# Kernel optimization log

Hardware: AMD Instinct MI355X
Metric: run time of the kernel (lower is better)

The kernel has to match this reference:

```python
import jax, jax.numpy as jnp
import numpy as np

HIDDEN = 2048
N_HEADS = 16
N_KV_HEADS = 8
HEAD_DIM = 128
MROPE_SECTION = [8, 8, 24, 24]          # sums to HEAD_DIM // 2
ROPE_THETA = 10000.0
B, S, CTX = 4, 1024, 2048
# per-frequency section index (which of the 4 position streams drives each freq)
_SEC_IDX = np.repeat(np.arange(len(MROPE_SECTION)), MROPE_SECTION)  # (HEAD_DIM//2,)


def setup_inputs() -> dict:
    key = jax.random.key(0)
    ks = jax.random.split(key, 6)
    return {
        "hidden_states": jax.random.normal(ks[0], (B, S, HIDDEN), jnp.float32),
        "Wqkv": jax.random.normal(ks[1], (HIDDEN, (N_HEADS + 2 * N_KV_HEADS) * HEAD_DIM), jnp.float32) * 0.02,
        "Wo": jax.random.normal(ks[2], (N_HEADS * HEAD_DIM, HIDDEN), jnp.float32) * 0.02,
        "ctx_k": jax.random.normal(ks[3], (B, CTX, N_KV_HEADS, HEAD_DIM), jnp.float32),
        "ctx_v": jax.random.normal(ks[4], (B, CTX, N_KV_HEADS, HEAD_DIM), jnp.float32),
        "position_ids": jax.random.randint(ks[5], (len(MROPE_SECTION), S), 0, CTX + S, jnp.int32),
    }


def _mrope_cos_sin(position_ids):
    # position_ids: (n_sections, S) int -> cos/sin of shape (S, HEAD_DIM)
    half = HEAD_DIM // 2
    inv_freq = 1.0 / (ROPE_THETA ** (jnp.arange(0, half, dtype=jnp.float32) * 2.0 / HEAD_DIM))
    freqs = position_ids.astype(jnp.float32)[:, :, None] * inv_freq[None, None, :]  # (4, S, half)
    sec = jnp.asarray(_SEC_IDX)[None, None, :]                                       # (1, 1, half)
    f = jnp.take_along_axis(freqs, jnp.broadcast_to(sec, (1,) + freqs.shape[1:]), axis=0)[0]  # (S, half)
    emb = jnp.concatenate([f, f], axis=-1)  # (S, HEAD_DIM)
    return jnp.cos(emb), jnp.sin(emb)


def _rotate_half(x):
    h = x.shape[-1] // 2
    return jnp.concatenate([-x[..., h:], x[..., :h]], axis=-1)


def reference(hidden_states, Wqkv, Wo, ctx_k, ctx_v, position_ids):
    b, s, _ = hidden_states.shape
    q_size = N_HEADS * HEAD_DIM
    kv_size = N_KV_HEADS * HEAD_DIM
    qkv = hidden_states @ Wqkv  # (B, S, q+2kv)
    q = qkv[..., :q_size].reshape(b, s, N_HEADS, HEAD_DIM)
    k = qkv[..., q_size:q_size + kv_size].reshape(b, s, N_KV_HEADS, HEAD_DIM)
    v = qkv[..., q_size + kv_size:].reshape(b, s, N_KV_HEADS, HEAD_DIM)

    cos, sin = _mrope_cos_sin(position_ids)        # (S, D) each
    cos = cos[None, :, None, :]
    sin = sin[None, :, None, :]
    q = q * cos + _rotate_half(q) * sin
    k = k * cos + _rotate_half(k) * sin

    # KV-cache concat along sequence dim
    k = jnp.concatenate([ctx_k, k], axis=1)        # (B, CTX+S, KV, D)
    v = jnp.concatenate([ctx_v, v], axis=1)

    # GQA: expand kv heads to query heads
    rep = N_HEADS // N_KV_HEADS
    k = jnp.repeat(k, rep, axis=2)                 # (B, T, H, D)
    v = jnp.repeat(v, rep, axis=2)

    scale = HEAD_DIM ** -0.5
    scores = jnp.einsum("bqhd,bkhd->bhqk", q, k) * scale  # non-causal
    probs = jax.nn.softmax(scores, axis=-1)
    out = jnp.einsum("bhqk,bkhd->bqhd", probs, v)  # (B, S, H, D)
    out = out.reshape(b, s, N_HEADS * HEAD_DIM)
    return out @ Wo
```

## Files before the change

### kernel.cpp

```cpp
#include <hip/hip_runtime.h>
#include <hip/hip_bf16.h>
#include <stdint.h>

#define NH 16
#define NKV 8
#define HD 128
#define BB 4
#define SS 1024
#define CTXL 2048
#define LT 3072
#define HID 2048
#define QKVN 4096
#define MROWS 4096

typedef __hip_bfloat16 bf16;
using f32x4 = __attribute__((ext_vector_type(4))) float;
using s16x8 = __attribute__((ext_vector_type(8))) short;

#define MFMA(a, b, c) __builtin_amdgcn_mfma_f32_16x16x32_bf16((a), (b), (c), 0, 0, 0)

__device__ __forceinline__ void gload_lds16(const void* g, void* l) {
  __builtin_amdgcn_global_load_lds((const __attribute__((address_space(1))) void*)g,
                                   (__attribute__((address_space(3))) void*)l, 16, 0, 0);
}

__device__ __forceinline__ void store_bf8(bf16* dst, const float* f) {
  bf16 tmp[8];
#pragma unroll
  for (int j = 0; j < 8; ++j) tmp[j] = __float2bfloat16(f[j]);
  __builtin_memcpy((void*)dst, (const void*)tmp, 16);
}

__device__ __forceinline__ float bf2f(short x) {
  unsigned int u = ((unsigned int)(unsigned short)x) << 16;
  float f;
  __builtin_memcpy(&f, &u, 4);
  return f;
}

#define P1_CVT 4096
#define P1_WQ (P1_CVT + 8192)
#define P1_WO (P1_WQ + 4096)
#define P1_RT (P1_WO + 256)
#define P1_CK (P1_RT + 4096)
#define P1_CV (P1_CK + 8192)

__global__ void prep1(const float* __restrict__ hs, const float* __restrict__ Wqkv,
                      const float* __restrict__ Wo, const float* __restrict__ ck,
                      const float* __restrict__ cv, const int* __restrict__ pid,
                      bf16* __restrict__ Hb, bf16* __restrict__ WqT,
                      bf16* __restrict__ WoT, bf16* __restrict__ Kf,
                      bf16* __restrict__ Vt, float* __restrict__ cosT,
                      float* __restrict__ sinT) {
  __shared__ float tile[32][33];
  const int blk = blockIdx.x, thr = threadIdx.x;
  if (blk < P1_CVT) {
    size_t tid = (size_t)blk * 256 + thr;
    const float4* p = (const float4*)(hs + tid * 8);
    float4 a = p[0], b = p[1];
    float f[8] = {a.x, a.y, a.z, a.w, b.x, b.y, b.z, b.w};
    store_bf8(Hb + tid * 8, f);
  } else if (blk < P1_WQ) {
    int j = blk - P1_CVT;
    int c0 = (j & 127) * 32, r0 = (j >> 7) * 32;
    int tx = thr & 31, ty = thr >> 5;
#pragma unroll
    for (int i = 0; i < 32; i += 8)
      tile[ty + i][tx] = Wqkv[(size_t)(r0 + ty + i) * QKVN + c0 + tx];
    __syncthreads();
#pragma unroll
    for (int i = 0; i < 32; i += 8)
      WqT[(size_t)(c0 + ty + i) * HID + r0 + tx] = __float2bfloat16(tile[tx][ty + i]);
  } else if (blk < P1_WO) {
    int j = blk - P1_WQ;
    int c0 = (j & 63) * 32, r0 = (j >> 6) * 32;
    int tx = thr & 31, ty = thr >> 5;
#pragma unroll
    for (int i = 0; i < 32; i += 8)
      tile[ty + i][tx] = Wo[(size_t)(r0 + ty + i) * 2048 + c0 + tx];
    __syncthreads();
#pragma unroll
    for (int i = 0; i < 32; i += 8)
      WoT[(size_t)(c0 + ty + i) * 2048 + r0 + tx] = __float2bfloat16(tile[tx][ty + i]);
  } else if (blk < P1_RT) {
    int tid = (blk - P1_WO) * 256 + thr;
    int j = tid & 63, s = tid >> 6;
    int sec = (j < 8) ? 0 : (j < 16) ? 1 : (j < 40) ? 2 : 3;
    float pos = (float)pid[sec * SS + s];
    float inv = __expf(-(float)j * 0.14391156831212787f);
    float a = pos * inv;
    cosT[tid] = cosf(a);
    sinT[tid] = sinf(a);
  } else if (blk < P1_CK) {
    int tid = (blk - P1_RT) * 256 + thr;
    int d8 = tid & 15, l = (tid >> 4) & 2047, h = (tid >> 15) & 7, b = tid >> 18;
    const float* s = ck + (((size_t)b * CTXL + l) * NKV + h) * HD + d8 * 8;
    const float4* p = (const float4*)s;
    float4 a = p[0], bb = p[1];
    float f[8] = {a.x, a.y, a.z, a.w, bb.x, bb.y, bb.z, bb.w};
    store_bf8(Kf + (((size_t)(b * NKV + h)) * LT + l) * HD + d8 * 8, f);
  } else {
    int j = blk - P1_CK;
    int l0 = (j & 63) * 32, d0 = ((j >> 6) & 3) * 32;
    int bz = j >> 8, b = bz >> 3, h = bz & 7;
    int tx = thr & 31, ty = thr >> 5;
#pragma unroll
    for (int i = 0; i < 32; i += 8)
      tile[ty + i][tx] =
          cv[(((size_t)b * CTXL + l0 + ty + i) * NKV + h) * HD + d0 + tx];
    __syncthreads();
#pragma unroll
    for (int i = 0; i < 32; i += 8)
      Vt[(((size_t)(b * NKV + h)) * HD + d0 + ty + i) * LT + l0 + tx] =
          __float2bfloat16(tile[tx][ty + i]);
  }
}

__global__ void prep2(const bf16* __restrict__ qkv, const float* __restrict__ cosT,
                      const float* __restrict__ sinT, bf16* __restrict__ Kf,
                      bf16* __restrict__ Vt) {
  __shared__ float tile[32][33];
  const int blk = blockIdx.x, thr = threadIdx.x;
  if (blk < 8192) {
    int tid = blk * 256 + thr;
    int j = tid & 63, h = (tid >> 6) & 7, s = (tid >> 9) & 1023, b = tid >> 19;
    const bf16* src = qkv + ((size_t)b * SS + s) * QKVN + 2048 + h * HD;
    float x1 = __bfloat162float(src[j]), x2 = __bfloat162float(src[j + 64]);
    float c = cosT[s * 64 + j], sn = sinT[s * 64 + j];
    bf16* dst = Kf + (((size_t)(b * NKV + h)) * LT + CTXL + s) * HD;
    dst[j] = __float2bfloat16(x1 * c - x2 * sn);
    dst[j + 64] = __float2bfloat16(x2 * c + x1 * sn);
  } else {
    int j = blk - 8192;
    int s0 = (j & 31) * 32, d0 = ((j >> 5) & 3) * 32;
    int bz = j >> 7, b = bz >> 3, h = bz & 7;
    int tx = thr & 31, ty = thr >> 5;
#pragma unroll
    for (int i = 0; i < 32; i += 8)
      tile[ty + i][tx] = __bfloat162float(
          qkv[((size_t)b * SS + s0 + ty + i) * QKVN + 3072 + h * HD + d0 + tx]);
    __syncthreads();
#pragma unroll
    for (int i = 0; i < 32; i += 8)
      Vt[(((size_t)(b * NKV + h)) * HD + d0 + ty + i) * LT + CTXL + s0 + tx] =
          __float2bfloat16(tile[tx][ty + i]);
  }
}

template <typename OT>
__global__ __launch_bounds__(512, 1) void gemm_bt(const bf16* __restrict__ A,
                                                  const bf16* __restrict__ BT,
                                                  OT* __restrict__ C, int M, int N,
                                                  int K) {
  __shared__ __attribute__((aligned(16))) bf16 lA[3][256][64];
  __shared__ __attribute__((aligned(16))) bf16 lB[3][128][64];
  const int t = threadIdx.x;
  const int lane = t & 63, w = t >> 6;
  const int wr = w >> 1, wc = w & 1;
  const int lrow = lane & 15, kgrp = lane >> 4;
  const int rchk = lrow & 7;
  const int lin = blockIdx.y * gridDim.x + blockIdx.x;
  const int qq = (gridDim.x * gridDim.y) >> 3;
  const int swz = (lin & 7) * qq + (lin >> 3);
  const int bx = swz % gridDim.x, by = swz / gridDim.x;
  const int m0 = by * 256, n0 = bx * 128;
  const int srow = lane >> 3;
  const int schk = (lane & 7) ^ srow;
  const f32x4 fz = {0.f, 0.f, 0.f, 0.f};
  f32x4 acc[4][4];
#pragma unroll
  for (int i = 0; i < 4; ++i)
#pragma unroll
    for (int j = 0; j < 4; ++j) acc[i][j] = fz;
  const int NTK = K >> 6;

#define GSTAGE(ib, kt)                                                      \
  do {                                                                      \
    _Pragma("unroll") for (int c = 0; c < 4; ++c) {                         \
      int ra = c * 64 + w * 8 + srow;                                       \
      gload_lds16(A + (size_t)(m0 + ra) * K + (kt)*64 + schk * 8,           \
                  &lA[ib][c * 64 + w * 8][0]);                              \
    }                                                                       \
    _Pragma("unroll") for (int c = 0; c < 2; ++c) {                         \
      int rb = c * 64 + w * 8 + srow;                                       \
      gload_lds16(BT + (size_t)(n0 + rb) * K + (kt)*64 + schk * 8,          \
                  &lB[ib][c * 64 + w * 8][0]);                              \
    }                                                                       \
  } while (0)

  GSTAGE(0, 0);
  GSTAGE(1, 1);
  int ib = 0;
  for (int kt = 0; kt < NTK; ++kt) {
    if (kt + 1 < NTK)
      asm volatile("s_waitcnt vmcnt(6) lgkmcnt(0)" ::: "memory");
    else
      asm volatile("s_waitcnt vmcnt(0) lgkmcnt(0)" ::: "memory");
    __builtin_amdgcn_s_barrier();
    __builtin_amdgcn_sched_barrier(0);
    if (kt + 2 < NTK) {
      int ib2 = ib + 2;
      if (ib2 >= 3) ib2 -= 3;
      GSTAGE(ib2, kt + 2);
    }
#pragma unroll
    for (int kk = 0; kk < 2; ++kk) {
      s16x8 af[4], bf[4];
#pragma unroll
      for (int i = 0; i < 4; ++i)
        af[i] = *(const s16x8*)&lA[ib][wr * 64 + i * 16 + lrow]
                                     [(((kk << 2) + kgrp) ^ rchk) * 8];
#pragma unroll
      for (int j = 0; j < 4; ++j)
        bf[j] = *(const s16x8*)&lB[ib][wc * 64 + j * 16 + lrow]
                                     [(((kk << 2) + kgrp) ^ rchk) * 8];
      __builtin_amdgcn_s_setprio(1);
#pragma unroll
      for (int i = 0; i < 4; ++i)
#pragma unroll
        for (int j = 0; j < 4; ++j) acc[i][j] = MFMA(af[i], bf[j], acc[i][j]);
      __builtin_amdgcn_s_setprio(0);
    }
    ++ib;
    if (ib >= 3) ib = 0;
  }
#undef GSTAGE

#pragma unroll
  for (int i = 0; i < 4; ++i)
#pragma unroll
    for (int j = 0; j < 4; ++j)
#pragma unroll
      for (int r = 0; r < 4; ++r) {
        int row = m0 + wr * 64 + i * 16 + kgrp * 4 + r;
        int col = n0 + wc * 64 + j * 16 + lrow;
        float v = acc[i][j][r];
        if constexpr (sizeof(OT) == 2)
          C[(size_t)row * N + col] = __float2bfloat16(v);
        else
          C[(size_t)row * N + col] = v;
      }
}


#define PSTR 72
#define KVB 128
#define NTT 24
#define SCALE2 0.1275174335919605f

__global__ __launch_bounds__(512, 2) void flash_attn(
    const bf16* __restrict__ qkv, const float* __restrict__ cosT,
    const float* __restrict__ sinT, const bf16* __restrict__ Kf,
    const bf16* __restrict__ Vt, bf16* __restrict__ O) {
  __shared__ __attribute__((aligned(16))) bf16 Kl[2][128][128];
  __shared__ __attribute__((aligned(16))) bf16 Vl[128][128];
  __shared__ __attribute__((aligned(16))) bf16 P_lds[8][32][PSTR];
  const int t = threadIdx.x, lane = t & 63, w = t >> 6;
  const int id = blockIdx.x;
  const int b = id >> 6, hk = id & 7;
  const int h = (hk << 1) | ((id >> 5) & 1);
  const int qb = (id >> 3) & 3;
  const int lrow = lane & 15, kgrp = lane >> 4;
  const bf16* Kp = Kf + (size_t)(b * NKV + hk) * LT * HD;
  const bf16* Vp = Vt + (size_t)(b * NKV + hk) * HD * LT;

  s16x8 qf[2][4];
#pragma unroll
  for (int f = 0; f < 2; ++f) {
    int srw_i = qb * 256 + w * 32 + f * 16 + lrow;
    const bf16* qrow = qkv + ((size_t)b * SS + srw_i) * QKVN + h * HD;
    s16x8 qr[4];
#pragma unroll
    for (int kd = 0; kd < 4; ++kd)
      qr[kd] = *(const s16x8*)&qrow[kd * 32 + kgrp * 8];
    const float* crow = cosT + srw_i * 64 + kgrp * 8;
    const float* srow = sinT + srw_i * 64 + kgrp * 8;
    float qv[4][8], cc[2][8], ssv[2][8];
#pragma unroll
    for (int kd = 0; kd < 4; ++kd)
#pragma unroll
      for (int j = 0; j < 8; ++j) qv[kd][j] = bf2f(qr[kd][j]);
#pragma unroll
    for (int g = 0; g < 2; ++g)
#pragma unroll
      for (int j = 0; j < 8; ++j) {
        cc[g][j] = crow[g * 32 + j];
        ssv[g][j] = srow[g * 32 + j];
      }
    bf16 o[4][8];
#pragma unroll
    for (int j = 0; j < 8; ++j) {
      o[0][j] = __float2bfloat16(qv[0][j] * cc[0][j] - qv[2][j] * ssv[0][j]);
      o[1][j] = __float2bfloat16(qv[1][j] * cc[1][j] - qv[3][j] * ssv[1][j]);
      o[2][j] = __float2bfloat16(qv[2][j] * cc[0][j] + qv[0][j] * ssv[0][j]);
      o[3][j] = __float2bfloat16(qv[3][j] * cc[1][j] + qv[1][j] * ssv[1][j]);
    }
#pragma unroll
    for (int kd = 0; kd < 4; ++kd) __builtin_memcpy(&qf[f][kd], o[kd], 16);
  }

  const f32x4 fz = {0.f, 0.f, 0.f, 0.f};
  f32x4 acc[2][8];
#pragma unroll
  for (int f = 0; f < 2; ++f)
#pragma unroll
    for (int i = 0; i < 8; ++i) acc[f][i] = fz;
  float m_[2] = {-1e30f, -1e30f}, l_[2] = {0.f, 0.f};

#define STAGE_K(buf, l0)                                                        \
  do {                                                                          \
    _Pragma("unroll") for (int c = 0; c < 4; ++c) {                             \
      int row = w * 16 + c * 4 + (lane >> 4);                                   \
      gload_lds16(Kp + (size_t)((l0) + row) * HD + ((lane & 15) ^ (row & 15)) * 8, \
                  &Kl[buf][w * 16 + c * 4][0]);                                 \
    }                                                                           \
  } while (0)
#define STAGE_V(l0)                                                             \
  do {                                                                          \
    _Pragma("unroll") for (int c = 0; c < 4; ++c) {                             \
      int d = w * 16 + c * 4 + (lane >> 4);                                     \
      gload_lds16(Vp + (size_t)d * LT + (l0) + ((lane & 15) ^ (d & 15)) * 8,    \
                  &Vl[w * 16 + c * 4][0]);                                      \
    }                                                                           \
  } while (0)

  STAGE_K(0, 0);
  __syncthreads();

  for (int tt = 0; tt < NTT; ++tt) {
    const int cur = tt & 1;
    STAGE_V(tt * KVB);
    if (tt + 1 < NTT) STAGE_K(cur ^ 1, (tt + 1) * KVB);

    f32x4 sc[2][8];
#pragma unroll
    for (int f = 0; f < 2; ++f)
#pragma unroll
      for (int cf = 0; cf < 8; ++cf) sc[f][cf] = fz;
#pragma unroll
    for (int cf = 0; cf < 8; ++cf)
#pragma unroll
      for (int kd = 0; kd < 4; ++kd) {
        s16x8 kb =
            *(const s16x8*)&Kl[cur][cf * 16 + lrow][((kd * 4 + kgrp) ^ lrow) * 8];
#pragma unroll
        for (int f = 0; f < 2; ++f) sc[f][cf] = MFMA(kb, qf[f][kd], sc[f][cf]);
      }

    float mxv[2];
#pragma unroll
    for (int f = 0; f < 2; ++f) {
      float mx = sc[f][0][0];
#pragma unroll
      for (int cf = 0; cf < 8; ++cf)
#pragma unroll
        for (int r = 0; r < 4; ++r) mx = fmaxf(mx, sc[f][cf][r]);
      mx *= SCALE2;
      mx = fmaxf(mx, __shfl_xor(mx, 16, 64));
      mx = fmaxf(mx, __shfl_xor(mx, 32, 64));
      mxv[f] = mx;
    }
    bool nb = (mxv[0] > m_[0] + 8.f) || (mxv[1] > m_[1] + 8.f);
    if (__any(nb)) {
#pragma unroll
      for (int f = 0; f < 2; ++f) {
        float mn = fmaxf(m_[f], mxv[f]);
        float so = exp2f(m_[f] - mn);
        m_[f] = mn;
        l_[f] *= so;
        float sob[4];
#pragma unroll
        for (int r = 0; r < 4; ++r) sob[r] = __shfl(so, kgrp * 4 + r, 16);
#pragma unroll
        for (int nd = 0; nd < 8; ++nd)
#pragma unroll
          for (int r = 0; r < 4; ++r) acc[f][nd][r] *= sob[r];
      }
    }

    float lp[2] = {0.f, 0.f};
#pragma unroll
    for (int f = 0; f < 2; ++f)
#pragma unroll
      for (int cf = 0; cf < 4; ++cf) {
        bf16 pk[4];
#pragma unroll
        for (int r = 0; r < 4; ++r) {
          float p = exp2f(sc[f][cf][r] * SCALE2 - m_[f]);
          lp[f] += p;
          pk[r] = __float2bfloat16(p);
        }
        __builtin_memcpy((void*)&P_lds[w][f * 16 + lrow][cf * 16 + kgrp * 4], pk, 8);
      }
    s16x8 pa[2][2];
#pragma unroll
    for (int f = 0; f < 2; ++f)
#pragma unroll
      for (int kc = 0; kc < 2; ++kc)
        pa[f][kc] = *(const s16x8*)&P_lds[w][f * 16 + lrow][kc * 32 + kgrp * 8];

    __syncthreads();

#pragma unroll
    for (int nd = 0; nd < 8; ++nd)
#pragma unroll
      for (int kc = 0; kc < 2; ++kc) {
        s16x8 vb = *(const s16x8*)&Vl[nd * 16 + lrow]
                                     [((kc * 4 + kgrp) ^ lrow) * 8];
#pragma unroll
        for (int f = 0; f < 2; ++f) acc[f][nd] = MFMA(pa[f][kc], vb, acc[f][nd]);
      }

#pragma unroll
    for (int f = 0; f < 2; ++f)
#pragma unroll
      for (int cf = 4; cf < 8; ++cf) {
        bf16 pk[4];
#pragma unroll
        for (int r = 0; r < 4; ++r) {
          float p = exp2f(sc[f][cf][r] * SCALE2 - m_[f]);
          lp[f] += p;
          pk[r] = __float2bfloat16(p);
        }
        __builtin_memcpy(
            (void*)&P_lds[w][f * 16 + lrow][(cf - 4) * 16 + kgrp * 4], pk, 8);
      }
#pragma unroll
    for (int f = 0; f < 2; ++f) {
      l_[f] += lp[f];
#pragma unroll
      for (int kc = 0; kc < 2; ++kc)
        pa[f][kc] = *(const s16x8*)&P_lds[w][f * 16 + lrow][kc * 32 + kgrp * 8];
    }
#pragma unroll
    for (int nd = 0; nd < 8; ++nd)
#pragma unroll
      for (int kc = 0; kc < 2; ++kc) {
        s16x8 vb = *(const s16x8*)&Vl[nd * 16 + lrow]
                                     [((8 + kc * 4 + kgrp) ^ lrow) * 8];
#pragma unroll
        for (int f = 0; f < 2; ++f) acc[f][nd] = MFMA(pa[f][kc], vb, acc[f][nd]);
      }
    __syncthreads();
  }
#undef STAGE_K
#undef STAGE_V

  float li[2][4];
#pragma unroll
  for (int f = 0; f < 2; ++f) {
    float lv = l_[f];
    lv += __shfl_xor(lv, 16, 64);
    lv += __shfl_xor(lv, 32, 64);
#pragma unroll
    for (int r = 0; r < 4; ++r) li[f][r] = 1.f / __shfl(lv, kgrp * 4 + r, 16);
  }
#pragma unroll
  for (int f = 0; f < 2; ++f)
#pragma unroll
    for (int nd = 0; nd < 8; ++nd)
#pragma unroll
      for (int r = 0; r < 4; ++r) {
        int row = qb * 256 + w * 32 + f * 16 + kgrp * 4 + r;
        O[((size_t)b * SS + row) * 2048 + h * HD + nd * 16 + lrow] =
            __float2bfloat16(acc[f][nd][r] * li[f][r]);
      }
}


extern "C" void kernel_launch(void* const* d_in, const int* in_sizes, int n_in,
                              void* d_out, int out_size, void* d_ws, size_t ws_size,
                              hipStream_t stream) {
  const float* hs = (const float*)d_in[0];
  const float* Wqkv = (const float*)d_in[1];
  const float* Wo = (const float*)d_in[2];
  const float* ctx_k = (const float*)d_in[3];
  const float* ctx_v = (const float*)d_in[4];
  const int* pid = (const int*)d_in[5];
  float* out = (float*)d_out;
  char* ws = (char*)d_ws;

  bf16* Hb = (bf16*)(ws);
  bf16* WqT = (bf16*)(ws + 16777216);
  bf16* WoT = (bf16*)(ws + 33554432);
  bf16* qkv = (bf16*)(ws + 41943040);
  bf16* Kfull = (bf16*)(ws + 92274688);
  bf16* Vt = (bf16*)(ws + 117440512);
  float* cosT = (float*)(ws + 142606336);
  float* sinT = (float*)(ws + 142606336 + 262144);
  bf16* attn = Hb;

  prep1<<<P1_CV, 256, 0, stream>>>(hs, Wqkv, Wo, ctx_k, ctx_v, pid, Hb, WqT, WoT,
                                   Kfull, Vt, cosT, sinT);
  gemm_bt<bf16><<<dim3(QKVN / 128, MROWS / 256), 512, 0, stream>>>(
      Hb, WqT, qkv, MROWS, QKVN, HID);
  prep2<<<12288, 256, 0, stream>>>(qkv, cosT, sinT, Kfull, Vt);
  flash_attn<<<256, 512, 0, stream>>>(qkv, cosT, sinT, Kfull, Vt, attn);
  gemm_bt<float><<<dim3(2048 / 128, MROWS / 256), 512, 0, stream>>>(
      attn, WoT, out, MROWS, 2048, HID);
}
```

Before: 325.8 us.

## Double-buffer V tiles and drop mid-iteration barrier in flash attention

V tiles now get their own double buffer in LDS and are prefetched one iteration ahead together with K, instead of being loaded at the start of the iteration that uses them. Because the current V tile is already resident, the `__syncthreads` between the two P·V halves is removed, and the two halves are folded into one loop. P staging is shrunk to one 16-row slab per wave, reused for both query fragments. This aims to hide V load latency and cut a block-wide barrier per tile, at the cost of a larger LDS footprint (about 146KB) that leaves little headroom.

```diff
diff --git a/kernel.cpp b/kernel.cpp
--- a/kernel.cpp
+++ b/kernel.cpp
@@ -253,8 +253,8 @@
     const float* __restrict__ sinT, const bf16* __restrict__ Kf,
     const bf16* __restrict__ Vt, bf16* __restrict__ O) {
   __shared__ __attribute__((aligned(16))) bf16 Kl[2][128][128];
-  __shared__ __attribute__((aligned(16))) bf16 Vl[128][128];
-  __shared__ __attribute__((aligned(16))) bf16 P_lds[8][32][PSTR];
+  __shared__ __attribute__((aligned(16))) bf16 Vl[2][128][128];
+  __shared__ __attribute__((aligned(16))) bf16 P_lds[8][16][PSTR];
   const int t = threadIdx.x, lane = t & 63, w = t >> 6;
   const int id = blockIdx.x;
   const int b = id >> 6, hk = id & 7;
@@ -315,22 +315,25 @@
                   &Kl[buf][w * 16 + c * 4][0]);                                 \
     }                                                                           \
   } while (0)
-#define STAGE_V(l0)                                                             \
+#define STAGE_V(buf, l0)                                                        \
   do {                                                                          \
     _Pragma("unroll") for (int c = 0; c < 4; ++c) {                             \
       int d = w * 16 + c * 4 + (lane >> 4);                                     \
       gload_lds16(Vp + (size_t)d * LT + (l0) + ((lane & 15) ^ (d & 15)) * 8,    \
-                  &Vl[w * 16 + c * 4][0]);                                      \
+                  &Vl[buf][w * 16 + c * 4][0]);                                 \
     }                                                                           \
   } while (0)
 
   STAGE_K(0, 0);
+  STAGE_V(0, 0);
   __syncthreads();
 
   for (int tt = 0; tt < NTT; ++tt) {
     const int cur = tt & 1;
-    STAGE_V(tt * KVB);
-    if (tt + 1 < NTT) STAGE_K(cur ^ 1, (tt + 1) * KVB);
+    if (tt + 1 < NTT) {
+      STAGE_K(cur ^ 1, (tt + 1) * KVB);
+      STAGE_V(cur ^ 1, (tt + 1) * KVB);
+    }
 
     f32x4 sc[2][8];
 #pragma unroll
@@ -380,67 +383,39 @@
 
     float lp[2] = {0.f, 0.f};
 #pragma unroll
-    for (int f = 0; f < 2; ++f)
-#pragma unroll
-      for (int cf = 0; cf < 4; ++cf) {
-        bf16 pk[4];
-#pragma unroll
-        for (int r = 0; r < 4; ++r) {
-          float p = exp2f(sc[f][cf][r] * SCALE2 - m_[f]);
-          lp[f] += p;
-          pk[r] = __float2bfloat16(p);
+    for (int half = 0; half < 2; ++half) {
+      s16x8 pa[2][2];
+#pragma unroll
+      for (int f = 0; f < 2; ++f) {
+#pragma unroll
+        for (int cf = 0; cf < 4; ++cf) {
+          int cfs = half * 4 + cf;
+          bf16 pk[4];
+#pragma unroll
+          for (int r = 0; r < 4; ++r) {
+            float p = exp2f(sc[f][cfs][r] * SCALE2 - m_[f]);
+            lp[f] += p;
+            pk[r] = __float2bfloat16(p);
+          }
+          __builtin_memcpy((void*)&P_lds[w][lrow][cf * 16 + kgrp * 4], pk, 8);
         }
-        __builtin_memcpy((void*)&P_lds[w][f * 16 + lrow][cf * 16 + kgrp * 4], pk, 8);
-      }
-    s16x8 pa[2][2];
-#pragma unroll
-    for (int f = 0; f < 2; ++f)
-#pragma unroll
-      for (int kc = 0; kc < 2; ++kc)
-        pa[f][kc] = *(const s16x8*)&P_lds[w][f * 16 + lrow][kc * 32 + kgrp * 8];
-
-    __syncthreads();
-
-#pragma unroll
-    for (int nd = 0; nd < 8; ++nd)
-#pragma unroll
-      for (int kc = 0; kc < 2; ++kc) {
-        s16x8 vb = *(const s16x8*)&Vl[nd * 16 + lrow]
-                                     [((kc * 4 + kgrp) ^ lrow) * 8];
-#pragma unroll
-        for (int f = 0; f < 2; ++f) acc[f][nd] = MFMA(pa[f][kc], vb, acc[f][nd]);
-      }
-
-#pragma unroll
-    for (int f = 0; f < 2; ++f)
-#pragma unroll
-      for (int cf = 4; cf < 8; ++cf) {
-        bf16 pk[4];
-#pragma unroll
-        for (int r = 0; r < 4; ++r) {
-          float p = exp2f(sc[f][cf][r] * SCALE2 - m_[f]);
-          lp[f] += p;
-          pk[r] = __float2bfloat16(p);
+#pragma unroll
+        for (int kc = 0; kc < 2; ++kc)
+          pa[f][kc] = *(const s16x8*)&P_lds[w][lrow][kc * 32 + kgrp * 8];
+      }
+#pragma unroll
+      for (int nd = 0; nd < 8; ++nd)
+#pragma unroll
+        for (int kc = 0; kc < 2; ++kc) {
+          s16x8 vb = *(const s16x8*)&Vl[cur][nd * 16 + lrow]
+                                       [((half * 8 + kc * 4 + kgrp) ^ lrow) * 8];
+#pragma unroll
+          for (int f = 0; f < 2; ++f) acc[f][nd] = MFMA(pa[f][kc], vb, acc[f][nd]);
         }
-        __builtin_memcpy(
-            (void*)&P_lds[w][f * 16 + lrow][(cf - 4) * 16 + kgrp * 4], pk, 8);
-      }
-#pragma unroll
-    for (int f = 0; f < 2; ++f) {
-      l_[f] += lp[f];
-#pragma unroll
-      for (int kc = 0; kc < 2; ++kc)
-        pa[f][kc] = *(const s16x8*)&P_lds[w][f * 16 + lrow][kc * 32 + kgrp * 8];
-    }
-#pragma unroll
-    for (int nd = 0; nd < 8; ++nd)
-#pragma unroll
-      for (int kc = 0; kc < 2; ++kc) {
-        s16x8 vb = *(const s16x8*)&Vl[nd * 16 + lrow]
-                                     [((8 + kc * 4 + kgrp) ^ lrow) * 8];
-#pragma unroll
-        for (int f = 0; f < 2; ++f) acc[f][nd] = MFMA(pa[f][kc], vb, acc[f][nd]);
-      }
+    }
+#pragma unroll
+    for (int f = 0; f < 2; ++f) l_[f] += lp[f];
+
     __syncthreads();
   }
 #undef STAGE_K
```

New measurement: 317.7 us. -2.5%, faster.
